# Performance work log

Hardware: AMD Instinct MI355X
Metric: run time of the kernel (lower is better)

## Reference

```python
import jax, jax.numpy as jnp
import numpy as np

N_PARENT = 16384
N_CHILD = 8 * N_PARENT  # nearest upsample, nempty=False: 8 children per parent
C = 128
K = 27  # 3x3x3 octree conv stencil


def setup_inputs() -> dict:
    key = jax.random.key(0)
    k1, k2, k3, k4 = jax.random.split(key, 4)
    x = jax.random.normal(k1, (N_PARENT, C), dtype=jnp.float32)
    # conv weight per stencil offset, fan-in scaled init
    w = jax.random.normal(k2, (K, C, C), dtype=jnp.float32) / np.sqrt(K * C)
    b = jnp.zeros((C,), dtype=jnp.float32)
    # neighbor table at depth+1; -1 marks missing neighbors (zero-padded)
    neigh = jax.random.randint(k3, (N_CHILD, K), -1, N_CHILD, dtype=jnp.int32)
    return {"x": x, "w": w, "b": b, "neigh": neigh}


def reference(x, w, b, neigh):
    # OctreeUpsample(nearest, nempty=False): copy each parent feature to its
    # 8 contiguous children at depth+1.
    xu = jnp.repeat(x, 8, axis=0)  # [N_child, C]
    # OctreeConv: gather 27 neighbors (missing -> 0), then GEMM + bias.
    valid = neigh >= 0  # [N_child, 27]
    g = jnp.where(valid[..., None], xu[jnp.clip(neigh, 0)], 0.0)  # [N_child, 27, C]
    out = jnp.einsum('nkc,kcd->nd', g, w) + b  # [N_child, C]
    return out
```

## Files before the change

kernel.cpp:

```cpp
#include <hip/hip_runtime.h>
#include <hip/hip_bf16.h>

#define N_PARENT 16384
#define N_CHILD (8 * N_PARENT)
#define CC 128
#define KK 27

#define BM 128
#define BN 128
#define BK 64

#define XB_OFF 0
#define XB_ELEMS (N_PARENT * CC)
#define WT_OFF XB_ELEMS
#define WT_ELEMS (KK * CC * CC)
#define ZR_OFF (WT_OFF + WT_ELEMS)
#define ZR_ELEMS 128
#define ZR_BYTE (ZR_OFF * 2)

typedef __attribute__((ext_vector_type(8))) __bf16 bf16x8;
typedef __attribute__((ext_vector_type(4))) float f32x4;

__device__ __forceinline__ void gll16(const void* g, void* l) {
  __builtin_amdgcn_global_load_lds(
      (const __attribute__((address_space(1))) unsigned int*)g,
      (__attribute__((address_space(3))) unsigned int*)l,
      16, 0, 0);
}

__global__ void prep_kernel(const float* __restrict__ x,
                            const float* __restrict__ w,
                            __hip_bfloat16* __restrict__ ws) {
  const int stride = gridDim.x * blockDim.x;
  const int tid = blockIdx.x * blockDim.x + threadIdx.x;
  for (int i = tid; i < XB_ELEMS; i += stride)
    ws[XB_OFF + i] = __float2bfloat16(x[i]);
  for (int j = tid; j < WT_ELEMS; j += stride) {
    const int k = j / (CC * CC);
    const int rem = j - k * CC * CC;
    const int d = rem >> 7;
    const int c = rem & 127;
    ws[WT_OFF + j] = __float2bfloat16(w[k * CC * CC + c * CC + d]);
  }
  if (tid < ZR_ELEMS) ws[ZR_OFF + tid] = __float2bfloat16(0.0f);
}

__global__ __launch_bounds__(256, 2) void upconv_kernel(
    const int* __restrict__ neigh,
    const __hip_bfloat16* __restrict__ ws,
    const float* __restrict__ bias,
    float* __restrict__ out) {
  __shared__ __align__(16) __hip_bfloat16 As[2][BM * BK];
  __shared__ __align__(16) __hip_bfloat16 Bs[2][BN * BK];
  __shared__ int ridx[BM * KK];

  const int tid = threadIdx.x;
  const int wv = tid >> 6;
  const int l = tid & 63;
  const int wr = wv >> 1;
  const int wc = wv & 1;
  const int row0 = blockIdx.x * BM;

  for (int j = tid; j < BM * KK; j += 256) {
    const int nv = neigh[row0 * KK + j];
    ridx[j] = (nv >= 0) ? ((nv >> 3) << 8) : ZR_BYTE;
  }
  __syncthreads();

  const int lr = l & 15;
  const int lk8 = (l >> 4) * 8;
  const int lrow = l >> 3;
  const int scol = ((l & 7) ^ lrow) * 8;
  const int sw = (lr & 7) * 8;
  const int aLaneB = scol * 2;

  const char* xbB = (const char*)(ws + XB_OFF);
  const __hip_bfloat16* wB = ws + WT_OFF + (wv * 32 + lrow) * CC + scol;

  f32x4 acc[4][4] = {};
  int roff[4];

  auto loadRid = [&](int k) {
#pragma unroll
    for (int i = 0; i < 4; ++i)
      roff[i] = ridx[(wv * 32 + i * 8 + lrow) * KK + k];
  };

  auto stageA = [&](int buf, int hb) {
#pragma unroll
    for (int i = 0; i < 4; ++i)
      gll16(xbB + roff[i] + hb + aLaneB, &As[buf][(wv * 32 + i * 8) * BK]);
  };
  auto stageB = [&](int buf, const __hip_bfloat16* wp) {
#pragma unroll
    for (int i = 0; i < 4; ++i)
      gll16(wp + i * 8 * CC, &Bs[buf][(wv * 32 + i * 8) * BK]);
  };

  auto compute = [&](int buf) {
    const __hip_bfloat16* ap = As[buf];
    const __hip_bfloat16* bp = Bs[buf];
#pragma unroll
    for (int kc = 0; kc < 2; ++kc) {
      const int ce = (kc * 32 + lk8) ^ sw;
      bf16x8 a[4], b[4];
#pragma unroll
      for (int m = 0; m < 4; ++m)
        a[m] = *reinterpret_cast<const bf16x8*>(
            &ap[(wr * 64 + m * 16 + lr) * BK + ce]);
#pragma unroll
      for (int n = 0; n < 4; ++n)
        b[n] = *reinterpret_cast<const bf16x8*>(
            &bp[(wc * 64 + n * 16 + lr) * BK + ce]);
      __builtin_amdgcn_s_setprio(1);
#pragma unroll
      for (int m = 0; m < 4; ++m)
#pragma unroll
        for (int n = 0; n < 4; ++n)
          acc[m][n] = __builtin_amdgcn_mfma_f32_16x16x32_bf16(
              a[m], b[n], acc[m][n], 0, 0, 0);
      __builtin_amdgcn_s_setprio(0);
    }
  };

  loadRid(0);
  stageB(0, wB);
  stageA(0, 0);

  for (int k = 0; k < KK; ++k) {
    stageB(1, wB + 64);
    stageA(1, 128);
    if (k + 1 < KK) loadRid(k + 1);
    asm volatile("s_waitcnt vmcnt(8)" ::: "memory");
    __builtin_amdgcn_s_barrier();
    compute(0);
    __builtin_amdgcn_s_barrier();

    wB += CC * CC;
    if (k + 1 < KK) {
      stageB(0, wB);
      stageA(0, 0);
      asm volatile("s_waitcnt vmcnt(8)" ::: "memory");
    } else {
      asm volatile("s_waitcnt vmcnt(0)" ::: "memory");
    }
    __builtin_amdgcn_s_barrier();
    compute(1);
    __builtin_amdgcn_s_barrier();
  }

  float bv[4];
#pragma unroll
  for (int n = 0; n < 4; ++n) bv[n] = bias[wc * 64 + n * 16 + lr];
  const int rbase = row0 + wr * 64 + (l >> 4) * 4;
#pragma unroll
  for (int m = 0; m < 4; ++m)
#pragma unroll
    for (int n = 0; n < 4; ++n)
#pragma unroll
      for (int q = 0; q < 4; ++q)
        out[(size_t)(rbase + m * 16 + q) * CC + wc * 64 + n * 16 + lr] =
            acc[m][n][q] + bv[n];
}

extern "C" void kernel_launch(void* const* d_in, const int* in_sizes, int n_in,
                              void* d_out, int out_size, void* d_ws,
                              size_t ws_size, hipStream_t stream) {
  const float* x = (const float*)d_in[0];
  const float* w = (const float*)d_in[1];
  const float* b = (const float*)d_in[2];
  const int* neigh = (const int*)d_in[3];
  __hip_bfloat16* ws = (__hip_bfloat16*)d_ws;
  float* out = (float*)d_out;

  hipLaunchKernelGGL(prep_kernel, dim3(512), dim3(256), 0, stream, x, w, ws);
  hipLaunchKernelGGL(upconv_kernel, dim3(N_CHILD / BM), dim3(256), 0, stream,
                     neigh, ws, b, out);
}
```

Before: 136.4 us.

## Halve K-tile to 32, use 16-bit neighbor indices, and target four blocks per CU

Shrinks the K tile from 64 to 32 so each stencil offset is processed in four smaller stages, and stores neighbor row indices as 16-bit values to cut LDS use. Together these let the kernel request four resident blocks per CU instead of two, aiming to hide gather latency through occupancy. The XOR swizzle on LDS is dropped, and each stage now issues fewer MFMAs between barriers, so bank conflicts and barrier overhead may rise.

```diff
diff --git a/kernel.cpp b/kernel.cpp
--- a/kernel.cpp
+++ b/kernel.cpp
@@ -8,7 +8,7 @@
 
 #define BM 128
 #define BN 128
-#define BK 64
+#define BK 32
 
 #define XB_OFF 0
 #define XB_ELEMS (N_PARENT * CC)
@@ -16,7 +16,7 @@
 #define WT_ELEMS (KK * CC * CC)
 #define ZR_OFF (WT_OFF + WT_ELEMS)
 #define ZR_ELEMS 128
-#define ZR_BYTE (ZR_OFF * 2)
+#define ZR_ROW 19840
 
 typedef __attribute__((ext_vector_type(8))) __bf16 bf16x8;
 typedef __attribute__((ext_vector_type(4))) float f32x4;
@@ -45,14 +45,14 @@
   if (tid < ZR_ELEMS) ws[ZR_OFF + tid] = __float2bfloat16(0.0f);
 }
 
-__global__ __launch_bounds__(256, 2) void upconv_kernel(
+__global__ __launch_bounds__(256, 4) void upconv_kernel(
     const int* __restrict__ neigh,
     const __hip_bfloat16* __restrict__ ws,
     const float* __restrict__ bias,
     float* __restrict__ out) {
   __shared__ __align__(16) __hip_bfloat16 As[2][BM * BK];
   __shared__ __align__(16) __hip_bfloat16 Bs[2][BN * BK];
-  __shared__ int ridx[BM * KK];
+  __shared__ unsigned short ridx[BM * KK];
 
   const int tid = threadIdx.x;
   const int wv = tid >> 6;
@@ -63,90 +63,98 @@
 
   for (int j = tid; j < BM * KK; j += 256) {
     const int nv = neigh[row0 * KK + j];
-    ridx[j] = (nv >= 0) ? ((nv >> 3) << 8) : ZR_BYTE;
+    ridx[j] = (unsigned short)((nv >= 0) ? (nv >> 3) : ZR_ROW);
   }
   __syncthreads();
 
   const int lr = l & 15;
   const int lk8 = (l >> 4) * 8;
-  const int lrow = l >> 3;
-  const int scol = ((l & 7) ^ lrow) * 8;
-  const int sw = (lr & 7) * 8;
-  const int aLaneB = scol * 2;
+  const int g16 = l >> 2;
+  const int lbA = (l & 3) * 16;
+  const int sB = g16 * 256 + lbA;
 
   const char* xbB = (const char*)(ws + XB_OFF);
-  const __hip_bfloat16* wB = ws + WT_OFF + (wv * 32 + lrow) * CC + scol;
+  const char* wp = (const char*)(ws + WT_OFF);
 
   f32x4 acc[4][4] = {};
-  int roff[4];
 
-  auto loadRid = [&](int k) {
-#pragma unroll
-    for (int i = 0; i < 4; ++i)
-      roff[i] = ridx[(wv * 32 + i * 8 + lrow) * KK + k];
+  const int ri0 = (wv * 32 + g16) * KK;
+  const int ri1 = (wv * 32 + 16 + g16) * KK;
+  int r0 = ((int)ridx[ri0]) << 8;
+  int r1 = ((int)ridx[ri1]) << 8;
+
+  auto stageA = [&](int buf, int qb, int a0, int a1) {
+    gll16(xbB + a0 + qb + lbA, &As[buf][(wv * 32) * BK]);
+    gll16(xbB + a1 + qb + lbA, &As[buf][(wv * 32 + 16) * BK]);
   };
-
-  auto stageA = [&](int buf, int hb) {
-#pragma unroll
-    for (int i = 0; i < 4; ++i)
-      gll16(xbB + roff[i] + hb + aLaneB, &As[buf][(wv * 32 + i * 8) * BK]);
-  };
-  auto stageB = [&](int buf, const __hip_bfloat16* wp) {
-#pragma unroll
-    for (int i = 0; i < 4; ++i)
-      gll16(wp + i * 8 * CC, &Bs[buf][(wv * 32 + i * 8) * BK]);
+  auto stageB = [&](int buf, const char* w, int qb) {
+    gll16(w + (wv * 32) * 256 + qb + sB, &Bs[buf][(wv * 32) * BK]);
+    gll16(w + (wv * 32 + 16) * 256 + qb + sB, &Bs[buf][(wv * 32 + 16) * BK]);
   };
 
   auto compute = [&](int buf) {
-    const __hip_bfloat16* ap = As[buf];
-    const __hip_bfloat16* bp = Bs[buf];
+    bf16x8 a[4], b[4];
 #pragma unroll
-    for (int kc = 0; kc < 2; ++kc) {
-      const int ce = (kc * 32 + lk8) ^ sw;
-      bf16x8 a[4], b[4];
+    for (int m = 0; m < 4; ++m)
+      a[m] = *reinterpret_cast<const bf16x8*>(
+          &As[buf][(wr * 64 + m * 16 + lr) * BK + lk8]);
 #pragma unroll
-      for (int m = 0; m < 4; ++m)
-        a[m] = *reinterpret_cast<const bf16x8*>(
-            &ap[(wr * 64 + m * 16 + lr) * BK + ce]);
+    for (int n = 0; n < 4; ++n)
+      b[n] = *reinterpret_cast<const bf16x8*>(
+          &Bs[buf][(wc * 64 + n * 16 + lr) * BK + lk8]);
+    __builtin_amdgcn_s_setprio(1);
+#pragma unroll
+    for (int m = 0; m < 4; ++m)
 #pragma unroll
       for (int n = 0; n < 4; ++n)
-        b[n] = *reinterpret_cast<const bf16x8*>(
-            &bp[(wc * 64 + n * 16 + lr) * BK + ce]);
-      __builtin_amdgcn_s_setprio(1);
-#pragma unroll
-      for (int m = 0; m < 4; ++m)
-#pragma unroll
-        for (int n = 0; n < 4; ++n)
-          acc[m][n] = __builtin_amdgcn_mfma_f32_16x16x32_bf16(
-              a[m], b[n], acc[m][n], 0, 0, 0);
-      __builtin_amdgcn_s_setprio(0);
-    }
+        acc[m][n] = __builtin_amdgcn_mfma_f32_16x16x32_bf16(
+            a[m], b[n], acc[m][n], 0, 0, 0);
+    __builtin_amdgcn_s_setprio(0);
   };
 
-  loadRid(0);
-  stageB(0, wB);
-  stageA(0, 0);
+#define WAITN(n) asm volatile("s_waitcnt vmcnt(" #n ")" ::: "memory")
+#define BAR() __builtin_amdgcn_s_barrier()
+
+  stageB(0, wp, 0);
+  stageA(0, 0, r0, r1);
 
   for (int k = 0; k < KK; ++k) {
-    stageB(1, wB + 64);
-    stageA(1, 128);
-    if (k + 1 < KK) loadRid(k + 1);
-    asm volatile("s_waitcnt vmcnt(8)" ::: "memory");
-    __builtin_amdgcn_s_barrier();
+    stageB(1, wp, 64);
+    stageA(1, 64, r0, r1);
+    WAITN(4); BAR();
     compute(0);
-    __builtin_amdgcn_s_barrier();
+    BAR();
 
-    wB += CC * CC;
+    stageB(0, wp, 128);
+    stageA(0, 128, r0, r1);
+    WAITN(4); BAR();
+    compute(1);
+    BAR();
+
+    stageB(1, wp, 192);
+    stageA(1, 192, r0, r1);
+    int n0 = r0, n1 = r1;
     if (k + 1 < KK) {
-      stageB(0, wB);
-      stageA(0, 0);
-      asm volatile("s_waitcnt vmcnt(8)" ::: "memory");
+      n0 = ((int)ridx[ri0 + k + 1]) << 8;
+      n1 = ((int)ridx[ri1 + k + 1]) << 8;
+    }
+    WAITN(4); BAR();
+    compute(0);
+    BAR();
+
+    wp += 2 * CC * CC;
+    if (k + 1 < KK) {
+      stageB(0, wp, 0);
+      stageA(0, 0, n0, n1);
+      WAITN(4);
     } else {
-      asm volatile("s_waitcnt vmcnt(0)" ::: "memory");
+      WAITN(0);
     }
-    __builtin_amdgcn_s_barrier();
+    BAR();
     compute(1);
-    __builtin_amdgcn_s_barrier();
+    BAR();
+
+    r0 = n0; r1 = n1;
   }
 
   float bv[4];
```

Measured after the change: 152.2 us. 11.6% more time.
